# Performance work log

Measured on AMD Instinct MI355X. Metric: run time of the kernel, lower is better.

The kernel has to match this reference:

```python
import jax, jax.numpy as jnp
import numpy as np

NEG_INF = -9e15
ALPHA = 0.2  # LeakyReLU negative slope


def build_adjacency(node_emb, k):
    # cosine-similarity top-k adjacency, rows scatter 1.0 at top-k columns
    norm = node_emb / jnp.linalg.norm(node_emb, axis=1, keepdims=True)
    sim = norm @ norm.T                      # [N, N]
    _, idx = jax.lax.top_k(sim, k)           # [N, k]
    N = sim.shape[0]
    rows = jnp.arange(N)[:, None]
    adj = jnp.zeros_like(sim).at[rows, idx].set(1.0)
    return adj


def reference(x, mask, node_emb, gat_W, gat_a, fp_W, fp_b, op_W, op_b, k):
    B, W, N = x.shape                         # n_features == node count N
    H, F, _ = gat_W.shape                     # n_heads, hidden_dim
    adj = build_adjacency(node_emb, k)        # [N, N]

    # feature projection: every node gets the same projected sample vector
    h0 = x.reshape(B * W, N) @ fp_W + fp_b    # [BW, F]
    h_in = jnp.broadcast_to(h0[:, None, :], (B * W, N, F))  # [BW, N, F]

    # per-head linear: torch Linear uses y = x @ W.T, gat_W is [H, out, in]
    h = jnp.einsum('bnf,hof->bhno', h_in, gat_W)            # [BW, H, N, F]

    # additive attention scores without materializing [N,N,2F] concat:
    # e[i,j] = leakyrelu(h_i . a1 + h_j . a2)
    a1, a2 = gat_a[:, :F], gat_a[:, F:]
    f1 = jnp.einsum('bhno,ho->bhn', h, a1)
    f2 = jnp.einsum('bhno,ho->bhn', h, a2)
    e = jax.nn.leaky_relu(f1[..., :, None] + f2[..., None, :], ALPHA)  # [BW,H,N,N]

    e = jnp.where(adj > 0, e, NEG_INF)
    attn = jax.nn.softmax(e, axis=-1)         # dropout is identity in eval mode
    h_prime = jax.nn.relu(jnp.einsum('bhnm,bhmo->bhno', attn, h))      # [BW,H,N,F]

    # concat heads along feature dim (head order matches torch cat)
    h_cat = jnp.transpose(h_prime, (0, 2, 1, 3)).reshape(B * W, N, H * F)
    imputed = h_cat @ op_W + op_b             # [BW, N, n_features]
    imputed = imputed.mean(axis=1).reshape(B, W, N)
    output = x * (1.0 - mask) + imputed * mask
    return output, adj


def setup_inputs() -> dict:
    key = jax.random.key(0)
    ks = jax.random.split(key, 8)
    B, Wn, N, F, H = 8, 64, 128, 128, 4
    s = 0.05
    return {
        'x': jax.random.normal(ks[0], (B, Wn, N), jnp.float32),
        'mask': jax.random.uniform(ks[1], (B, Wn, N), jnp.float32),
        'node_emb': jax.random.normal(ks[2], (N, F), jnp.float32),
        'gat_W': jax.random.normal(ks[3], (H, F, F), jnp.float32) * s,
        'gat_a': jax.random.normal(ks[4], (H, 2 * F), jnp.float32) * s,
        'fp_W': jax.random.normal(ks[5], (N, F), jnp.float32) * s,
        'fp_b': jnp.zeros((F,), jnp.float32),
        'op_W': jax.random.normal(ks[6], (H * F, N), jnp.float32) * s,
        'op_b': jnp.zeros((N,), jnp.float32),
        'k': 30,
    }
```

## Files before the change

### kernel.cpp

```cpp
#include <hip/hip_runtime.h>

#define BW   512
#define NN   128
#define FF   128
#define HH   4
#define HF   512
#define ROWS 4
#define MAINB (BW / ROWS)
#define ADJR 4
#define ADJB (NN / ADJR)
#define NT   512

__global__ void __launch_bounds__(NT)
fused_kernel(const float* __restrict__ x,
             const float* __restrict__ mask,
             const float* __restrict__ emb,
             const float* __restrict__ gatW,
             const float* __restrict__ fpW,
             const float* __restrict__ fpb,
             const float* __restrict__ opW,
             const float* __restrict__ opb,
             const int*   __restrict__ kptr,
             float* __restrict__ out_main,
             float* __restrict__ out_adj) {
    const int b = blockIdx.x;
    const int u = threadIdx.x;

    __shared__ float sx  [ROWS][NN];
    __shared__ float sh  [ROWS][FF];
    __shared__ float srg [ROWS][HF];
    __shared__ float psum[4][ROWS][NN];
    __shared__ float s_emb[NN][FF + 1];
    __shared__ float s_np [NN][4];
    __shared__ float s_nrm[NN];
    __shared__ float s_sim[ADJR][NN];

    if (b < MAINB) {
        const int r0 = b * ROWS;
        sx[u >> 7][u & 127] = x[r0 * NN + u];
        __syncthreads();

        {
            const int ng = u >> 7;
            const int o  = u & 127;
            float a0 = 0.f, a1 = 0.f, a2 = 0.f, a3 = 0.f;
            const int n0 = ng * 32;
            #pragma unroll 8
            for (int nn = 0; nn < 32; ++nn) {
                const int n = n0 + nn;
                const float w = fpW[n * FF + o];
                a0 = fmaf(sx[0][n], w, a0);
                a1 = fmaf(sx[1][n], w, a1);
                a2 = fmaf(sx[2][n], w, a2);
                a3 = fmaf(sx[3][n], w, a3);
            }
            psum[ng][0][o] = a0; psum[ng][1][o] = a1;
            psum[ng][2][o] = a2; psum[ng][3][o] = a3;
        }
        __syncthreads();
        {
            const int rr = u >> 7, o = u & 127;
            sh[rr][o] = fpb[o] + psum[0][rr][o] + psum[1][rr][o]
                                + psum[2][rr][o] + psum[3][rr][o];
        }
        __syncthreads();

        {
            float acc0 = 0.f, acc1 = 0.f, acc2 = 0.f, acc3 = 0.f;
            const float4* __restrict__ gw = (const float4*)(gatW + (size_t)u * FF);
            #pragma unroll 4
            for (int f4 = 0; f4 < FF / 4; ++f4) {
                const float4 w = gw[f4];
                const int f = f4 * 4;
                acc0 = fmaf(sh[0][f], w.x, fmaf(sh[0][f+1], w.y, fmaf(sh[0][f+2], w.z, fmaf(sh[0][f+3], w.w, acc0))));
                acc1 = fmaf(sh[1][f], w.x, fmaf(sh[1][f+1], w.y, fmaf(sh[1][f+2], w.z, fmaf(sh[1][f+3], w.w, acc1))));
                acc2 = fmaf(sh[2][f], w.x, fmaf(sh[2][f+1], w.y, fmaf(sh[2][f+2], w.z, fmaf(sh[2][f+3], w.w, acc2))));
                acc3 = fmaf(sh[3][f], w.x, fmaf(sh[3][f+1], w.y, fmaf(sh[3][f+2], w.z, fmaf(sh[3][f+3], w.w, acc3))));
            }
            srg[0][u] = fmaxf(acc0, 0.f);
            srg[1][u] = fmaxf(acc1, 0.f);
            srg[2][u] = fmaxf(acc2, 0.f);
            srg[3][u] = fmaxf(acc3, 0.f);
        }
        __syncthreads();

        {
            const int cg = u >> 7;
            const int j  = u & 127;
            float a0 = 0.f, a1 = 0.f, a2 = 0.f, a3 = 0.f;
            const int t0 = cg * 128;
            #pragma unroll 8
            for (int tt = 0; tt < 128; ++tt) {
                const int t = t0 + tt;
                const float w = opW[t * NN + j];
                a0 = fmaf(srg[0][t], w, a0);
                a1 = fmaf(srg[1][t], w, a1);
                a2 = fmaf(srg[2][t], w, a2);
                a3 = fmaf(srg[3][t], w, a3);
            }
            psum[cg][0][j] = a0; psum[cg][1][j] = a1;
            psum[cg][2][j] = a2; psum[cg][3][j] = a3;
        }
        __syncthreads();
        {
            const int rr = u >> 7, j = u & 127;
            const float val = opb[j] + psum[0][rr][j] + psum[1][rr][j]
                                      + psum[2][rr][j] + psum[3][rr][j];
            const int idx = (r0 + rr) * NN + j;
            const float m = mask[idx];
            out_main[idx] = x[idx] * (1.f - m) + val * m;
        }
    } else {
        const int i0 = (b - MAINB) * ADJR;
        const int k  = *kptr;

        {
            const float4* __restrict__ e4 = (const float4*)emb;
            #pragma unroll
            for (int it = 0; it < (NN * FF / 4) / NT; ++it) {
                const int e = it * NT + u;
                const float4 v = e4[e];
                const int row = e >> 5;
                const int c4  = (e & 31) * 4;
                s_emb[row][c4 + 0] = v.x;
                s_emb[row][c4 + 1] = v.y;
                s_emb[row][c4 + 2] = v.z;
                s_emb[row][c4 + 3] = v.w;
            }
        }
        __syncthreads();

        {
            const int row = u >> 2, part = u & 3;
            float s = 0.f;
            const int f0 = part * 32;
            #pragma unroll 8
            for (int f = 0; f < 32; ++f) {
                const float e = s_emb[row][f0 + f];
                s = fmaf(e, e, s);
            }
            s_np[row][part] = s;
        }
        __syncthreads();
        if (u < NN)
            s_nrm[u] = sqrtf(s_np[u][0] + s_np[u][1] + s_np[u][2] + s_np[u][3]);
        __syncthreads();
        #pragma unroll
        for (int it = 0; it < (NN * FF) / NT; ++it) {
            const int e = it * NT + u;
            const int row = e >> 7, col = e & 127;
            s_emb[row][col] /= s_nrm[row];
        }
        __syncthreads();

        {
            const int g = u >> 7;
            const int j = u & 127;
            const int i = i0 + g;
            float d = 0.f;
            #pragma unroll 8
            for (int f = 0; f < FF; ++f)
                d = fmaf(s_emb[i][f], s_emb[j][f], d);
            s_sim[g][j] = d;
        }
        __syncthreads();

        {
            const int g = u >> 7;
            const int j = u & 127;
            const float my = s_sim[g][j];
            int rank = 0;
            #pragma unroll 8
            for (int m = 0; m < NN; ++m) {
                const float sm = s_sim[g][m];
                rank += (sm > my) | ((sm == my) & (m < j));
            }
            out_adj[(i0 + g) * NN + j] = (rank < k) ? 1.f : 0.f;
        }
    }
}

extern "C" void kernel_launch(void* const* d_in, const int* in_sizes, int n_in,
                              void* d_out, int out_size, void* d_ws, size_t ws_size,
                              hipStream_t stream) {
    const float* x        = (const float*)d_in[0];
    const float* mask     = (const float*)d_in[1];
    const float* node_emb = (const float*)d_in[2];
    const float* gat_W    = (const float*)d_in[3];
    const float* fp_W     = (const float*)d_in[5];
    const float* fp_b     = (const float*)d_in[6];
    const float* op_W     = (const float*)d_in[7];
    const float* op_b     = (const float*)d_in[8];
    const int*   kptr     = (const int*)d_in[9];

    float* out_main = (float*)d_out;
    float* out_adj  = (float*)d_out + BW * NN;

    fused_kernel<<<MAINB + ADJB, NT, 0, stream>>>(
        x, mask, node_emb, gat_W, fp_W, fp_b, op_W, op_b, kptr,
        out_main, out_adj);
}
```

Measured before the change: 85.44 us.

## Transpose shared staging to float4, rebalance adjacency blocks, apply norms post-dot

Stores the per-row activations transposed so each shared read yields all four rows as one float4. The GAT and output projections now compute two output columns per thread, which reuses each shared read across more FMAs and halves redundant weight loads. The adjacency path uses two rows per block across twice as many blocks and splits both the dot product and the rank count across thread halves. It divides by the norms after the dot product instead of normalising the whole embedding matrix. A shared-memory union cuts LDS footprint. Risks include only half the threads working in the GAT stage and small floating-point differences in similarity that could change tie-breaking in top-k.

```diff
diff --git a/kernel.cpp b/kernel.cpp
--- a/kernel.cpp
+++ b/kernel.cpp
@@ -1,15 +1,30 @@
 #include <hip/hip_runtime.h>
 
-#define BW   512
-#define NN   128
-#define FF   128
-#define HH   4
-#define HF   512
-#define ROWS 4
-#define MAINB (BW / ROWS)
-#define ADJR 4
-#define ADJB (NN / ADJR)
-#define NT   512
+#define BW    512
+#define NN    128
+#define FF    128
+#define HF    512
+#define ROWS  4
+#define MAINB 128
+#define ADJR  2
+#define ADJB  64
+#define NT    512
+
+union SMem {
+    struct {
+        float sxT [NN][4];
+        float shT [FF][4];
+        float srgT[HF][4];
+        float ps  [8][ROWS][NN];
+    } m;
+    struct {
+        float emb[NN][FF + 1];
+        float nrm[NN];
+        float ps2[ADJR][2][NN];
+        float sim[ADJR][NN];
+        int   rnk[2][ADJR][NN];
+    } a;
+};
 
 __global__ void __launch_bounds__(NT)
 fused_kernel(const float* __restrict__ x,
@@ -23,159 +38,171 @@
              const int*   __restrict__ kptr,
              float* __restrict__ out_main,
              float* __restrict__ out_adj) {
+    __shared__ SMem sm;
     const int b = blockIdx.x;
     const int u = threadIdx.x;
 
-    __shared__ float sx  [ROWS][NN];
-    __shared__ float sh  [ROWS][FF];
-    __shared__ float srg [ROWS][HF];
-    __shared__ float psum[4][ROWS][NN];
-    __shared__ float s_emb[NN][FF + 1];
-    __shared__ float s_np [NN][4];
-    __shared__ float s_nrm[NN];
-    __shared__ float s_sim[ADJR][NN];
-
     if (b < MAINB) {
         const int r0 = b * ROWS;
-        sx[u >> 7][u & 127] = x[r0 * NN + u];
-        __syncthreads();
-
-        {
-            const int ng = u >> 7;
-            const int o  = u & 127;
+
+        {
+            const int rr = u >> 7, n = u & 127;
+            sm.m.sxT[n][rr] = x[(r0 + rr) * NN + n];
+        }
+        __syncthreads();
+
+        {
+            const int g = u >> 7;
+            const int o = u & 127;
             float a0 = 0.f, a1 = 0.f, a2 = 0.f, a3 = 0.f;
-            const int n0 = ng * 32;
+            const int n0 = g * 32;
             #pragma unroll 8
             for (int nn = 0; nn < 32; ++nn) {
                 const int n = n0 + nn;
                 const float w = fpW[n * FF + o];
-                a0 = fmaf(sx[0][n], w, a0);
-                a1 = fmaf(sx[1][n], w, a1);
-                a2 = fmaf(sx[2][n], w, a2);
-                a3 = fmaf(sx[3][n], w, a3);
-            }
-            psum[ng][0][o] = a0; psum[ng][1][o] = a1;
-            psum[ng][2][o] = a2; psum[ng][3][o] = a3;
+                const float4 sv = *(const float4*)sm.m.sxT[n];
+                a0 = fmaf(sv.x, w, a0);
+                a1 = fmaf(sv.y, w, a1);
+                a2 = fmaf(sv.z, w, a2);
+                a3 = fmaf(sv.w, w, a3);
+            }
+            sm.m.ps[g][0][o] = a0; sm.m.ps[g][1][o] = a1;
+            sm.m.ps[g][2][o] = a2; sm.m.ps[g][3][o] = a3;
         }
         __syncthreads();
         {
             const int rr = u >> 7, o = u & 127;
-            sh[rr][o] = fpb[o] + psum[0][rr][o] + psum[1][rr][o]
-                                + psum[2][rr][o] + psum[3][rr][o];
-        }
-        __syncthreads();
-
-        {
-            float acc0 = 0.f, acc1 = 0.f, acc2 = 0.f, acc3 = 0.f;
-            const float4* __restrict__ gw = (const float4*)(gatW + (size_t)u * FF);
+            float s = fpb[o];
+            #pragma unroll
+            for (int g = 0; g < 4; ++g) s += sm.m.ps[g][rr][o];
+            sm.m.shT[o][rr] = s;
+        }
+        __syncthreads();
+
+        if (u < 256) {
+            const float4* __restrict__ w1 = (const float4*)(gatW + (size_t)u * FF);
+            const float4* __restrict__ w2 = (const float4*)(gatW + (size_t)(u + 256) * FF);
+            float b0 = 0.f, b1 = 0.f, b2 = 0.f, b3 = 0.f;
+            float c0 = 0.f, c1 = 0.f, c2 = 0.f, c3 = 0.f;
             #pragma unroll 4
             for (int f4 = 0; f4 < FF / 4; ++f4) {
-                const float4 w = gw[f4];
-                const int f = f4 * 4;
-                acc0 = fmaf(sh[0][f], w.x, fmaf(sh[0][f+1], w.y, fmaf(sh[0][f+2], w.z, fmaf(sh[0][f+3], w.w, acc0))));
-                acc1 = fmaf(sh[1][f], w.x, fmaf(sh[1][f+1], w.y, fmaf(sh[1][f+2], w.z, fmaf(sh[1][f+3], w.w, acc1))));
-                acc2 = fmaf(sh[2][f], w.x, fmaf(sh[2][f+1], w.y, fmaf(sh[2][f+2], w.z, fmaf(sh[2][f+3], w.w, acc2))));
-                acc3 = fmaf(sh[3][f], w.x, fmaf(sh[3][f+1], w.y, fmaf(sh[3][f+2], w.z, fmaf(sh[3][f+3], w.w, acc3))));
-            }
-            srg[0][u] = fmaxf(acc0, 0.f);
-            srg[1][u] = fmaxf(acc1, 0.f);
-            srg[2][u] = fmaxf(acc2, 0.f);
-            srg[3][u] = fmaxf(acc3, 0.f);
-        }
-        __syncthreads();
-
-        {
-            const int cg = u >> 7;
-            const int j  = u & 127;
-            float a0 = 0.f, a1 = 0.f, a2 = 0.f, a3 = 0.f;
-            const int t0 = cg * 128;
-            #pragma unroll 8
-            for (int tt = 0; tt < 128; ++tt) {
+                const float4 q1 = w1[f4];
+                const float4 q2 = w2[f4];
+                const float4 s0 = *(const float4*)sm.m.shT[f4 * 4 + 0];
+                const float4 s1 = *(const float4*)sm.m.shT[f4 * 4 + 1];
+                const float4 s2 = *(const float4*)sm.m.shT[f4 * 4 + 2];
+                const float4 s3 = *(const float4*)sm.m.shT[f4 * 4 + 3];
+                b0 = fmaf(s0.x, q1.x, fmaf(s1.x, q1.y, fmaf(s2.x, q1.z, fmaf(s3.x, q1.w, b0))));
+                b1 = fmaf(s0.y, q1.x, fmaf(s1.y, q1.y, fmaf(s2.y, q1.z, fmaf(s3.y, q1.w, b1))));
+                b2 = fmaf(s0.z, q1.x, fmaf(s1.z, q1.y, fmaf(s2.z, q1.z, fmaf(s3.z, q1.w, b2))));
+                b3 = fmaf(s0.w, q1.x, fmaf(s1.w, q1.y, fmaf(s2.w, q1.z, fmaf(s3.w, q1.w, b3))));
+                c0 = fmaf(s0.x, q2.x, fmaf(s1.x, q2.y, fmaf(s2.x, q2.z, fmaf(s3.x, q2.w, c0))));
+                c1 = fmaf(s0.y, q2.x, fmaf(s1.y, q2.y, fmaf(s2.y, q2.z, fmaf(s3.y, q2.w, c1))));
+                c2 = fmaf(s0.z, q2.x, fmaf(s1.z, q2.y, fmaf(s2.z, q2.z, fmaf(s3.z, q2.w, c2))));
+                c3 = fmaf(s0.w, q2.x, fmaf(s1.w, q2.y, fmaf(s2.w, q2.z, fmaf(s3.w, q2.w, c3))));
+            }
+            float4* dst1 = (float4*)sm.m.srgT[u];
+            float4* dst2 = (float4*)sm.m.srgT[u + 256];
+            *dst1 = make_float4(fmaxf(b0, 0.f), fmaxf(b1, 0.f), fmaxf(b2, 0.f), fmaxf(b3, 0.f));
+            *dst2 = make_float4(fmaxf(c0, 0.f), fmaxf(c1, 0.f), fmaxf(c2, 0.f), fmaxf(c3, 0.f));
+        }
+        __syncthreads();
+
+        {
+            const int cg = u >> 6;
+            const int jj = u & 63;
+            float a00 = 0.f, a01 = 0.f, a02 = 0.f, a03 = 0.f;
+            float a10 = 0.f, a11 = 0.f, a12 = 0.f, a13 = 0.f;
+            const int t0 = cg * 64;
+            #pragma unroll 8
+            for (int tt = 0; tt < 64; ++tt) {
                 const int t = t0 + tt;
-                const float w = opW[t * NN + j];
-                a0 = fmaf(srg[0][t], w, a0);
-                a1 = fmaf(srg[1][t], w, a1);
-                a2 = fmaf(srg[2][t], w, a2);
-                a3 = fmaf(srg[3][t], w, a3);
-            }
-            psum[cg][0][j] = a0; psum[cg][1][j] = a1;
-            psum[cg][2][j] = a2; psum[cg][3][j] = a3;
+                const float4 sv = *(const float4*)sm.m.srgT[t];
+                const float w0 = opW[t * NN + jj];
+                const float w1 = opW[t * NN + jj + 64];
+                a00 = fmaf(sv.x, w0, a00); a01 = fmaf(sv.y, w0, a01);
+                a02 = fmaf(sv.z, w0, a02); a03 = fmaf(sv.w, w0, a03);
+                a10 = fmaf(sv.x, w1, a10); a11 = fmaf(sv.y, w1, a11);
+                a12 = fmaf(sv.z, w1, a12); a13 = fmaf(sv.w, w1, a13);
+            }
+            sm.m.ps[cg][0][jj] = a00; sm.m.ps[cg][1][jj] = a01;
+            sm.m.ps[cg][2][jj] = a02; sm.m.ps[cg][3][jj] = a03;
+            sm.m.ps[cg][0][jj + 64] = a10; sm.m.ps[cg][1][jj + 64] = a11;
+            sm.m.ps[cg][2][jj + 64] = a12; sm.m.ps[cg][3][jj + 64] = a13;
         }
         __syncthreads();
         {
             const int rr = u >> 7, j = u & 127;
-            const float val = opb[j] + psum[0][rr][j] + psum[1][rr][j]
-                                      + psum[2][rr][j] + psum[3][rr][j];
+            float val = opb[j];
+            #pragma unroll
+            for (int g = 0; g < 8; ++g) val += sm.m.ps[g][rr][j];
             const int idx = (r0 + rr) * NN + j;
-            const float m = mask[idx];
-            out_main[idx] = x[idx] * (1.f - m) + val * m;
+            const float xv = x[idx];
+            const float mv = mask[idx];
+            out_main[idx] = fmaf(mv, val - xv, xv);
         }
     } else {
         const int i0 = (b - MAINB) * ADJR;
         const int k  = *kptr;
 
-        {
-            const float4* __restrict__ e4 = (const float4*)emb;
-            #pragma unroll
-            for (int it = 0; it < (NN * FF / 4) / NT; ++it) {
-                const int e = it * NT + u;
-                const float4 v = e4[e];
-                const int row = e >> 5;
-                const int c4  = (e & 31) * 4;
-                s_emb[row][c4 + 0] = v.x;
-                s_emb[row][c4 + 1] = v.y;
-                s_emb[row][c4 + 2] = v.z;
-                s_emb[row][c4 + 3] = v.w;
-            }
-        }
-        __syncthreads();
-
-        {
-            const int row = u >> 2, part = u & 3;
-            float s = 0.f;
-            const int f0 = part * 32;
-            #pragma unroll 8
-            for (int f = 0; f < 32; ++f) {
-                const float e = s_emb[row][f0 + f];
-                s = fmaf(e, e, s);
-            }
-            s_np[row][part] = s;
-        }
-        __syncthreads();
-        if (u < NN)
-            s_nrm[u] = sqrtf(s_np[u][0] + s_np[u][1] + s_np[u][2] + s_np[u][3]);
-        __syncthreads();
         #pragma unroll
         for (int it = 0; it < (NN * FF) / NT; ++it) {
             const int e = it * NT + u;
-            const int row = e >> 7, col = e & 127;
-            s_emb[row][col] /= s_nrm[row];
-        }
-        __syncthreads();
-
-        {
-            const int g = u >> 7;
-            const int j = u & 127;
-            const int i = i0 + g;
+            sm.a.emb[e >> 7][e & 127] = emb[e];
+        }
+        __syncthreads();
+        if (u < NN) {
+            float s = 0.f;
+            #pragma unroll 8
+            for (int f = 0; f < FF; ++f) {
+                const float e = sm.a.emb[u][f];
+                s = fmaf(e, e, s);
+            }
+            sm.a.nrm[u] = sqrtf(s);
+        }
+        __syncthreads();
+        {
+            const int g  = u >> 8;
+            const int fs = (u >> 7) & 1;
+            const int j  = u & 127;
+            const int i  = i0 + g;
+            const int f0 = fs * 64;
             float d = 0.f;
             #pragma unroll 8
-            for (int f = 0; f < FF; ++f)
-                d = fmaf(s_emb[i][f], s_emb[j][f], d);
-            s_sim[g][j] = d;
-        }
-        __syncthreads();
-
-        {
-            const int g = u >> 7;
-            const int j = u & 127;
-            const float my = s_sim[g][j];
-            int rank = 0;
-            #pragma unroll 8
-            for (int m = 0; m < NN; ++m) {
-                const float sm = s_sim[g][m];
-                rank += (sm > my) | ((sm == my) & (m < j));
-            }
-            out_adj[(i0 + g) * NN + j] = (rank < k) ? 1.f : 0.f;
+            for (int f = 0; f < 64; ++f)
+                d = fmaf(sm.a.emb[i][f0 + f], sm.a.emb[j][f0 + f], d);
+            sm.a.ps2[g][fs][j] = d;
+        }
+        __syncthreads();
+        if (u < 256) {
+            const int g = u >> 7, j = u & 127;
+            const float d = sm.a.ps2[g][0][j] + sm.a.ps2[g][1][j];
+            sm.a.sim[g][j] = d / (sm.a.nrm[i0 + g] * sm.a.nrm[j]);
+        }
+        __syncthreads();
+        {
+            const int g  = u >> 8;
+            const int ms = (u >> 7) & 1;
+            const int j  = u & 127;
+            const float my = sm.a.sim[g][j];
+            const int m0 = ms * 64;
+            int r = 0;
+            #pragma unroll 4
+            for (int m4 = 0; m4 < 16; ++m4) {
+                const int m = m0 + m4 * 4;
+                const float4 sv = *(const float4*)&sm.a.sim[g][m];
+                r += (sv.x > my) | ((sv.x == my) & (m + 0 < j));
+                r += (sv.y > my) | ((sv.y == my) & (m + 1 < j));
+                r += (sv.z > my) | ((sv.z == my) & (m + 2 < j));
+                r += (sv.w > my) | ((sv.w == my) & (m + 3 < j));
+            }
+            sm.a.rnk[ms][g][j] = r;
+        }
+        __syncthreads();
+        if (u < 256) {
+            const int g = u >> 7, j = u & 127;
+            const int r = sm.a.rnk[0][g][j] + sm.a.rnk[1][g][j];
+            out_adj[(i0 + g) * NN + j] = (r < k) ? 1.f : 0.f;
         }
     }
 }
```

Measured after the change: 85.73 us. Within noise of the previous version (+0.3%).
